# Performance work log

Measured on AMD Instinct MI355X. Metric: run time of the kernel, lower is better.

## Reference

```python
import jax, jax.numpy as jnp
import numpy as np
from jax import lax

NEG = -1e30  # safe -inf surrogate (avoids nan grads)
CTC_WEIGHT = 0.3


def _excl_cumsum(e):
    # exclusive cumsum along last axis: (..., U) -> (..., U+1)
    c = jnp.cumsum(e, axis=-1)
    return jnp.concatenate([jnp.zeros_like(c[..., :1]), c], axis=-1)


def _rnnt_loss(log_probs, targets, frame_len, tgt_len, blank):
    """RNNT forward DP. log_probs: (B,T,U+1,V) log-softmaxed. Returns per-seq NLL (B,)."""
    B, T, U1, V = log_probs.shape
    blank_lp = log_probs[..., blank]  # (B,T,U1)
    emit = jnp.take_along_axis(log_probs[:, :, :U1 - 1, :],
                               targets[:, None, :, None], axis=3)[..., 0]  # (B,T,U)
    # alpha[0,u] = sum_{j<u} emit[0,j]
    alpha0 = _excl_cumsum(emit[:, 0])  # (B,U1)

    def step(alpha_prev, inp):
        blank_prev, emit_t = inp  # (B,U1), (B,U)
        a = alpha_prev + blank_prev
        # alpha[t,u] = LSE(a_u, alpha[t,u-1] + emit[t,u-1]) solved in closed form:
        # alpha[t,u] = E[u] + cumLSE_{k<=u}(a_k - E[k]),  E = exclusive cumsum of emit
        E = _excl_cumsum(emit_t)
        alpha_t = E + lax.associative_scan(jnp.logaddexp, a - E, axis=-1)
        return alpha_t, alpha_t

    xs = (jnp.swapaxes(blank_lp[:, :-1], 0, 1), jnp.swapaxes(emit[:, 1:], 0, 1))
    _, alphas = lax.scan(step, alpha0, xs)
    alphas = jnp.concatenate([alpha0[None], alphas], axis=0)  # (T,B,U1)
    bi = jnp.arange(B)
    t_idx = frame_len - 1
    ll = alphas[t_idx, bi, tgt_len] + blank_lp[bi, t_idx, tgt_len]
    return -ll


def _ctc_loss(log_probs, targets, frame_len, tgt_len, blank):
    """CTC forward DP. log_probs: (B,T,V) log-softmaxed. Returns per-seq NLL (B,)."""
    B, T, V = log_probs.shape
    U = targets.shape[1]
    S = 2 * U + 1
    ext = jnp.full((B, S), blank, dtype=targets.dtype).at[:, 1::2].set(targets)  # (B,S)
    lp_ext = jnp.take_along_axis(log_probs, ext[:, None, :], axis=2)  # (B,T,S)
    ext_m2 = jnp.pad(ext[:, :-2], ((0, 0), (2, 0)), constant_values=blank)
    can_skip = (jnp.arange(S)[None, :] >= 2) & (ext != blank) & (ext != ext_m2)
    alpha0 = jnp.full((B, S), NEG).at[:, 0].set(lp_ext[:, 0, 0]).at[:, 1].set(lp_ext[:, 0, 1])

    def step(alpha, lp_t):
        p1 = jnp.pad(alpha[:, :-1], ((0, 0), (1, 0)), constant_values=NEG)
        p2 = jnp.where(can_skip,
                       jnp.pad(alpha[:, :-2], ((0, 0), (2, 0)), constant_values=NEG), NEG)
        m = jnp.maximum(jnp.maximum(alpha, p1), p2)
        new = lp_t + m + jnp.log(jnp.exp(alpha - m) + jnp.exp(p1 - m) + jnp.exp(p2 - m))
        return new, new

    _, alphas = lax.scan(step, alpha0, jnp.swapaxes(lp_ext, 0, 1)[1:])
    alphas = jnp.concatenate([alpha0[None], alphas], axis=0)  # (T,B,S)
    bi = jnp.arange(B)
    t_idx = frame_len - 1
    a_last = alphas[t_idx, bi, 2 * tgt_len]
    a_prev = alphas[t_idx, bi, 2 * tgt_len - 1]
    return -jnp.logaddexp(a_last, a_prev)


def setup_inputs() -> dict:
    key = jax.random.key(0)
    ks = jax.random.split(key, 9)
    B, T, U, V = 4, 200, 50, 1024
    D, H = 512, 640
    return {
        "x_enc": jax.random.normal(ks[0], (B, T, D), jnp.float32),
        "x_dec": jax.random.normal(ks[1], (B, U + 1, H), jnp.float32),
        "target": jax.random.randint(ks[2], (B, U), 0, V - 1),  # excludes blank = V-1
        "frame_length": jax.random.randint(ks[3], (B,), 150, T + 1).astype(jnp.int32),
        "target_length": jax.random.randint(ks[4], (B,), 30, U + 1).astype(jnp.int32),
        "W_ctc": jax.random.normal(ks[5], (D, V), jnp.float32) * 0.02,
        "b_ctc": jnp.zeros((V,), jnp.float32),
        "W_enc": jax.random.normal(ks[6], (D, H), jnp.float32) * 0.02,
        "W_pred": jax.random.normal(ks[7], (H, H), jnp.float32) * 0.02,
        "b_joint": jnp.zeros((H,), jnp.float32),
        "W_out": jax.random.normal(ks[8], (H, V), jnp.float32) * 0.02,
        "b_out": jnp.zeros((V,), jnp.float32),
    }


def reference(x_enc, x_dec, target, frame_length, target_length,
              W_ctc, b_ctc, W_enc, W_pred, b_joint, W_out, b_out):
    B = x_enc.shape[0]
    V = W_ctc.shape[1]
    blank = V - 1
    # CTC head: linear + log_softmax over vocab
    ctc_lp = jax.nn.log_softmax(x_enc @ W_ctc + b_ctc, axis=-1)  # (B,T,V)
    # Joiner: enc proj (B,T,1,J) + pred proj (B,1,U+1,J) -> tanh -> vocab
    joint = jnp.tanh(jnp.einsum('btd,dj->btj', x_enc, W_enc)[:, :, None, :]
                     + jnp.einsum('buh,hj->buj', x_dec, W_pred)[:, None, :, :]
                     + b_joint)  # (B,T,U+1,J)
    rnnt_lp = jax.nn.log_softmax(jnp.einsum('btuj,jv->btuv', joint, W_out) + b_out, axis=-1)
    rnnt = _rnnt_loss(rnnt_lp, target, frame_length, target_length, blank).mean()
    ctc = _ctc_loss(ctc_lp, target, frame_length, target_length, blank).sum() / B
    return rnnt + CTC_WEIGHT * ctc
```

## Files before the change

### kernel.cpp

```cpp
#include <hip/hip_runtime.h>
#include <hip/hip_bf16.h>

typedef __bf16 bf16_t;
typedef __attribute__((ext_vector_type(8))) __bf16 bf16x8;
typedef __attribute__((ext_vector_type(4))) float f32x4;
typedef __attribute__((ext_vector_type(8))) int i32x8;
typedef __attribute__((ext_vector_type(4))) int i32x4;

#define NEGV (-1e30f)

#define BB 4
#define TT 200
#define UU 50
#define U1 51
#define VV 1024
#define DD 512
#define HH 640
#define RTOT (BB*TT*U1)
#define RPAD 40832
#define NBLK 638
#define SS 101

__device__ __forceinline__ float lae(float a, float b) {
    float mx = fmaxf(a, b);
    return mx + __logf(__expf(a - mx) + __expf(b - mx));
}
__device__ __forceinline__ float lae3(float a, float b, float c) {
    float mx = fmaxf(fmaxf(a, b), c);
    return mx + __logf(__expf(a - mx) + __expf(b - mx) + __expf(c - mx));
}
__device__ __forceinline__ float tanh_fast(float x) {
    float ex = __expf(2.f * x);
    return 1.f - 2.f / (ex + 1.f);
}
__device__ __forceinline__ float tanh_rcp(float x) {
    x = fminf(fmaxf(x, -10.f), 10.f);
    float ex = __expf(2.f * x);
    float r = __builtin_amdgcn_rcpf(ex + 1.f);
    return (ex - 1.f) * r;
}

__device__ __forceinline__ void pack_seg(const float* __restrict__ W, bf16_t* __restrict__ Wf,
                                         int e, int K32, int N)
{
    int j  = e & 7;
    int l  = (e >> 3) & 63;
    int kk = (e >> 9) % K32;
    int nt = e / (K32 * 512);
    int v = nt * 16 + (l & 15);
    int k = kk * 32 + ((l >> 4) << 2) + (j & 3) + ((j >> 2) << 4);
    Wf[e] = (bf16_t)W[(size_t)k * N + v];
}

__device__ __forceinline__ void pack_out8_mx(const float* __restrict__ W, unsigned* __restrict__ Wf8,
                                             int e32)
{
    int w4   = e32 & 7;
    int l    = (e32 >> 3) & 63;
    int ksnt = e32 >> 9;
    int ks   = ksnt % 5;
    int nt   = ksnt / 5;
    int v = nt * 16 + (l & 15);
    int kb = ks * 128 + ((l >> 4) << 5) + w4 * 4;
    float f[4];
#pragma unroll
    for (int t = 0; t < 4; ++t) f[t] = W[(size_t)(kb + t) * VV + v] * 16.f;
    unsigned r = __builtin_amdgcn_cvt_pk_fp8_f32(f[0], f[1], 0, false);
    r = __builtin_amdgcn_cvt_pk_fp8_f32(f[2], f[3], r, true);
    Wf8[e32] = r;
}

__global__ void pack_all(const float* __restrict__ Wout, const float* __restrict__ Wenc,
                         const float* __restrict__ Wpred, const float* __restrict__ Wctc,
                         unsigned* __restrict__ FOut8, bf16_t* __restrict__ FEnc,
                         bf16_t* __restrict__ FPred, bf16_t* __restrict__ FCtc)
{
    int e = blockIdx.x * 256 + threadIdx.x;
    if (e < 163840) { pack_out8_mx(Wout, FOut8, e); return; }
    e -= 163840;
    if (e < 327680) { pack_seg(Wenc, FEnc, e, 16, 640); return; }
    e -= 327680;
    if (e < 409600) { pack_seg(Wpred, FPred, e, 20, 640); return; }
    e -= 409600;
    pack_seg(Wctc, FCtc, e, 16, 1024);
}

template<int K32, int L, bool LSE, int J>
__device__ void gemm_dev(const float* __restrict__ A, int M, int rowbase, int K,
                         const bf16_t* __restrict__ Wf, const float* __restrict__ bias,
                         float* __restrict__ C, float* __restrict__ lse_out, int N,
                         bf16_t* Atile, float (*ps)[8])
{
    const int tid = threadIdx.x;
#pragma unroll
    for (int it = 0; it < J * K32 / 8; ++it) {
        int fi = it * 512 + tid;
        int l = fi & 63, jk = fi >> 6;
        int j = jk / K32, kk = jk - j * K32;
        int row = rowbase + j * 16 + (l & 15);
        if (row > M - 1) row = M - 1;
        int c0 = kk * 32 + ((l >> 4) << 2);
        const float4 a0 = *(const float4*)&A[(size_t)row * K + c0];
        const float4 a1 = *(const float4*)&A[(size_t)row * K + c0 + 16];
        bf16x8 v;
        v[0] = (bf16_t)a0.x; v[1] = (bf16_t)a0.y; v[2] = (bf16_t)a0.z; v[3] = (bf16_t)a0.w;
        v[4] = (bf16_t)a1.x; v[5] = (bf16_t)a1.y; v[6] = (bf16_t)a1.z; v[7] = (bf16_t)a1.w;
        *(bf16x8*)&Atile[(size_t)fi * 8] = v;
    }
    __syncthreads();

    const int l = tid & 63, w = tid >> 6;
    const int lrow = l & 15, lhi = l >> 4;

    f32x4 acc[J][L];
#pragma unroll
    for (int j = 0; j < J; ++j)
#pragma unroll
        for (int li = 0; li < L; ++li) acc[j][li] = f32x4{0.f, 0.f, 0.f, 0.f};

    for (int kk = 0; kk < K32; ++kk) {
        bf16x8 a[J];
#pragma unroll
        for (int j = 0; j < J; ++j)
            a[j] = *(const bf16x8*)&Atile[(size_t)(((j * K32 + kk) * 64 + l) * 8)];
#pragma unroll
        for (int li = 0; li < L; ++li) {
            bf16x8 b = *(const bf16x8*)&Wf[(size_t)(((w * L + li) * K32 + kk) * 64 + l) * 8];
#pragma unroll
            for (int j = 0; j < J; ++j)
                acc[j][li] = __builtin_amdgcn_mfma_f32_16x16x32_bf16(a[j], b, acc[j][li], 0, 0, 0);
        }
    }

    float se[J][4];
    if (LSE) {
#pragma unroll
        for (int j = 0; j < J; ++j)
#pragma unroll
            for (int i = 0; i < 4; ++i) se[j][i] = 0.f;
    }
#pragma unroll
    for (int j = 0; j < J; ++j)
#pragma unroll
        for (int li = 0; li < L; ++li) {
            int col = (w * L + li) * 16 + lrow;
            float bv = bias ? bias[col] : 0.f;
#pragma unroll
            for (int i = 0; i < 4; ++i) {
                int grow = rowbase + 16 * j + lhi * 4 + i;
                float x = acc[j][li][i] + bv;
                if (grow < M) C[(size_t)grow * N + col] = x;
                if (LSE) se[j][i] += __expf(x);
            }
        }
    if (LSE) {
#pragma unroll
        for (int d = 1; d < 16; d <<= 1)
#pragma unroll
            for (int j = 0; j < J; ++j)
#pragma unroll
                for (int i = 0; i < 4; ++i) se[j][i] += __shfl_xor(se[j][i], d);
        if (lrow == 0) {
#pragma unroll
            for (int j = 0; j < J; ++j)
#pragma unroll
                for (int i = 0; i < 4; ++i) ps[16 * j + lhi * 4 + i][w] = se[j][i];
        }
        __syncthreads();
        if (tid < J * 16) {
            float s = 0.f;
#pragma unroll
            for (int w0 = 0; w0 < 8; ++w0) s += ps[tid][w0];
            int grow = rowbase + tid;
            if (grow < M) lse_out[grow] = __logf(s);
        }
    }
}

__global__ __launch_bounds__(512)
void mfma_gemm3(const float* __restrict__ x_enc, const float* __restrict__ x_dec,
                const bf16_t* __restrict__ FEnc, const bf16_t* __restrict__ FPred,
                const bf16_t* __restrict__ FCtc, const float* __restrict__ b_ctc,
                float* __restrict__ enc_proj, float* __restrict__ pred_proj,
                float* __restrict__ ctc_logits, float* __restrict__ ctc_lse)
{
    __shared__ bf16_t Atile[40960];
    __shared__ float ps[64][8];
    int blk = blockIdx.x;
    if (blk < 13)
        gemm_dev<16, 5, false, 4>(x_enc, 800, blk * 64, 512, FEnc, nullptr, enc_proj, nullptr, 640, Atile, ps);
    else if (blk < 17)
        gemm_dev<20, 5, false, 4>(x_dec, 204, (blk - 13) * 64, 640, FPred, nullptr, pred_proj, nullptr, 640, Atile, ps);
    else
        gemm_dev<16, 8, true, 4>(x_enc, 800, (blk - 17) * 64, 512, FCtc, b_ctc, ctc_logits, ctc_lse, 1024, Atile, ps);
}

__global__ __launch_bounds__(256)
void build_joint(const float* __restrict__ enc, const float* __restrict__ pred,
                 const float* __restrict__ bj, char* __restrict__ FA8)
{
    __shared__ __align__(16) char tile[64 * 656];
    __shared__ const float* ep[64];
    __shared__ const float* pp[64];
    const int blk = blockIdx.x;
    const int tid = threadIdx.x;

    if (tid < 64) {
        int r = blk * 64 + tid; if (r > RTOT - 1) r = RTOT - 1;
        int b = r / (TT * U1); int rem = r - b * (TT * U1);
        int t = rem / U1;      int u = rem - t * U1;
        ep[tid] = enc + (size_t)(b * TT + t) * HH;
        pp[tid] = pred + (size_t)(b * U1 + u) * HH;
    }
    __syncthreads();

#pragma unroll 4
    for (int it = 0; it < 40; ++it) {
        int i = it * 256 + tid;
        int row = i / 160;
        int c4 = i - row * 160;
        int c0 = c4 * 4;
        const float4 e4 = *(const float4*)&ep[row][c0];
        const float4 p4 = *(const float4*)&pp[row][c0];
        const float4 q4 = *(const float4*)&bj[c0];
        float f0 = tanh_rcp(e4.x + p4.x + q4.x);
        float f1 = tanh_rcp(e4.y + p4.y + q4.y);
        float f2 = tanh_rcp(e4.z + p4.z + q4.z);
        float f3 = tanh_rcp(e4.w + p4.w + q4.w);
        unsigned r0 = __builtin_amdgcn_cvt_pk_fp8_f32(f0, f1, 0, false);
        unsigned v = __builtin_amdgcn_cvt_pk_fp8_f32(f2, f3, r0, true);
        *(unsigned*)&tile[row * 656 + c0] = v;
    }
    __syncthreads();

#pragma unroll
    for (int it = 0; it < 10; ++it) {
        int c = it * 256 + tid;
        int lA = c & 63;
        int plane = c >> 6;
        int h = plane & 1;
        int jks = plane >> 1;
        int ks = jks % 5;
        int j = jks / 5;
        int row = j * 16 + (lA & 15);
        int kbase = ks * 128 + ((lA >> 4) << 5) + h * 16;
        uint4 v = *(const uint4*)&tile[row * 656 + kbase];
        *(uint4*)&FA8[(size_t)blk * 40960 + (size_t)c * 16] = v;
    }
}

__global__ __launch_bounds__(512)
void joint_gemm(const char* __restrict__ FA8,
                const unsigned* __restrict__ Wf8,
                const float* __restrict__ bo,
                const int* __restrict__ target,
                float* __restrict__ blank_buf, float* __restrict__ emit_buf)
{
    __shared__ __align__(16) char smbuf[40960];
    char* Afrag8 = smbuf;
    const int tid = threadIdx.x;
    const int blk = blockIdx.x;

    const int l = tid & 63, w = tid >> 6;
    const int lrow = l & 15, lhi = l >> 4;

    const uint4* src = (const uint4*)(FA8 + (size_t)blk * 40960);
#pragma unroll
    for (int it = 0; it < 5; ++it) {
        int c = it * 512 + tid;
        *(uint4*)&Afrag8[(size_t)c * 16] = src[c];
    }
    __syncthreads();

    f32x4 acc[4][8];
#pragma unroll
    for (int j = 0; j < 4; ++j)
#pragma unroll
        for (int li = 0; li < 8; ++li) acc[j][li] = f32x4{0.f, 0.f, 0.f, 0.f};

    const char* Bp8 = (const char*)Wf8 + (size_t)(w * 8) * 10240 + (size_t)l * 32;

    const int rot = blk % 5;
    auto kstep = [&](int ks) {
        i32x8 a[4];
#pragma unroll
        for (int j = 0; j < 4; ++j) {
            i32x4 lo = *(const i32x4*)(Afrag8 + (size_t)(((j * 5 + ks) * 2 + 0) * 1024 + l * 16));
            i32x4 hi = *(const i32x4*)(Afrag8 + (size_t)(((j * 5 + ks) * 2 + 1) * 1024 + l * 16));
            a[j][0] = lo[0]; a[j][1] = lo[1]; a[j][2] = lo[2]; a[j][3] = lo[3];
            a[j][4] = hi[0]; a[j][5] = hi[1]; a[j][6] = hi[2]; a[j][7] = hi[3];
        }
#pragma unroll
        for (int li = 0; li < 8; ++li) {
            i32x8 b = *(const i32x8*)(Bp8 + (size_t)li * 10240 + (size_t)ks * 2048);
#pragma unroll
            for (int j = 0; j < 4; ++j)
                acc[j][li] = __builtin_amdgcn_mfma_scale_f32_16x16x128_f8f6f4(
                    a[j], b, acc[j][li], 0, 0,
                    0, 0x7F7F7F7F, 0, 0x7F7F7F7F);
        }
    };
    for (int ks0 = rot; ks0 < 5; ++ks0) kstep(ks0);
    for (int ks0 = 0; ks0 < rot; ++ks0) kstep(ks0);

    int tg[4][4];
#pragma unroll
    for (int j = 0; j < 4; ++j)
#pragma unroll
        for (int i = 0; i < 4; ++i) {
            int r = blk * 64 + 16 * j + lhi * 4 + i; if (r > RTOT - 1) r = RTOT - 1;
            int b = r / (TT * U1); int rem = r - b * (TT * U1);
            int u = rem % U1;
            tg[j][i] = (u < UU) ? target[b * UU + u] : -1;
        }

    float se[4][4], ee[4][4], bbv[4][4];
#pragma unroll
    for (int j = 0; j < 4; ++j)
#pragma unroll
        for (int i = 0; i < 4; ++i) { se[j][i] = 0.f; ee[j][i] = NEGV; bbv[j][i] = NEGV; }

#pragma unroll
    for (int li = 0; li < 8; ++li) {
        int col = (w * 8 + li) * 16 + lrow;
        float bv = bo[col];
#pragma unroll
        for (int j = 0; j < 4; ++j)
#pragma unroll
            for (int i = 0; i < 4; ++i) {
                float x = acc[j][li][i] * 0.0625f + bv;
                se[j][i] += __expf(x);
                if (col == tg[j][i]) ee[j][i] = x;
            }
    }
    if (w == 7) {
        float bv = bo[1023];
#pragma unroll
        for (int j = 0; j < 4; ++j)
#pragma unroll
            for (int i = 0; i < 4; ++i) {
                float x = acc[j][7][i] * 0.0625f + bv;
                if (lrow == 15) bbv[j][i] = x;
            }
    }
#pragma unroll
    for (int d = 1; d < 16; d <<= 1)
#pragma unroll
        for (int j = 0; j < 4; ++j)
#pragma unroll
            for (int i = 0; i < 4; ++i) {
                se[j][i] += __shfl_xor(se[j][i], d);
                ee[j][i] = fmaxf(ee[j][i], __shfl_xor(ee[j][i], d));
                bbv[j][i] = fmaxf(bbv[j][i], __shfl_xor(bbv[j][i], d));
            }

    __syncthreads();
    float (*ps)[8] = (float (*)[8])(smbuf);
    float (*pe)[8] = (float (*)[8])(smbuf + 2048);
    float (*pb)[8] = (float (*)[8])(smbuf + 4096);
    if (lrow == 0) {
#pragma unroll
        for (int j = 0; j < 4; ++j)
#pragma unroll
            for (int i = 0; i < 4; ++i) {
                int r = 16 * j + lhi * 4 + i;
                ps[r][w] = se[j][i]; pe[r][w] = ee[j][i]; pb[r][w] = bbv[j][i];
            }
    }
    __syncthreads();
    if (tid < 64) {
        float s = 0.f, e = NEGV, bq = NEGV;
#pragma unroll
        for (int w0 = 0; w0 < 8; ++w0) {
            s += ps[tid][w0];
            e = fmaxf(e, pe[tid][w0]);
            bq = fmaxf(bq, pb[tid][w0]);
        }
        float lse = __logf(s);
        int gid = blk * 64 + tid;
        if (gid < RTOT) {
            blank_buf[gid] = bq - lse;
            emit_buf[gid]  = e - lse;
        }
    }
}

__global__ __launch_bounds__(256)
void dp_fused(const float* __restrict__ blank_buf, const float* __restrict__ emit_buf,
              const float* __restrict__ ctc_logits, const float* __restrict__ ctc_lse,
              const int* __restrict__ target, const int* __restrict__ frame_len,
              const int* __restrict__ tgt_len,
              float* __restrict__ out)
{
    __shared__ __align__(16) float sm[28416];
    const int bid = blockIdx.x;
    const int tid = threadIdx.x;

    if (bid < 4) {
        const int b = bid;
        float2* pk = (float2*)sm;
        for (int i = tid; i < TT * U1; i += 256) {
            int t = i / U1, uu = i - t * U1;
            float bl = blank_buf[(b * TT + t) * U1 + uu];
            float em = emit_buf[(b * TT + t) * U1 + uu];
            pk[uu * 217 + t + 8] = make_float2(bl, em);
        }
        __syncthreads();
        if (tid >= 64) return;
        const int u = tid;
        const int fl = frame_len[b], tl = tgt_len[b];
        const int dh = fl - 1 + tl;
        const bool isTL = (u == tl);
        const bool act = (u < U1);
        float A = (u == 0) ? 0.f : NEGV;
        float Asave = (dh == 0 && isTL) ? A : NEGV;
        const float2* prow = pk + u * 217;

        for (int d0 = 1; d0 <= 249; d0 += 8) {
            int tb = d0 - 1 - u;
            int tc = tb; if (tc < -8) tc = -8; if (tc > 200) tc = 200;
            float2 buf[8];
#pragma unroll
            for (int s = 0; s < 8; ++s) buf[s] = prow[tc + 8 + s];
#pragma unroll
            for (int s = 0; s < 8; ++s) {
                int d = d0 + s;
                int t_new = d - u;
                float2 be = buf[s];
                float vshare = A + be.y;
                float left = __shfl_up(vshare, 1);
                if (u == 0) left = NEGV;
                float up = (t_new >= 1) ? (A + be.x) : NEGV;
                float Anew = lae(up, left);
                bool valid = act && (t_new >= 0) && (t_new < TT);
                A = valid ? Anew : A;
                Asave = (isTL && d == dh) ? A : Asave;
            }
        }
        if (isTL && act) {
            float bl = prow[(fl - 1) + 8].x;
            atomicAdd(out, -0.25f * (Asave + bl));
        }
    } else {
        const int b = bid - 4;
        float* lpE = sm;
        float* lpO = sm + 208;
        for (int i = tid; i < TT; i += 256) {
            int bt = b * TT + i;
            lpE[i] = ctc_logits[(size_t)bt * VV + (VV - 1)] - ctc_lse[bt];
        }
        for (int i = tid; i < TT * UU; i += 256) {
            int t = i / UU, uu = i - t * UU;
            int bt = b * TT + t;
            lpO[uu * 209 + t] = ctc_logits[(size_t)bt * VV + target[b * UU + uu]] - ctc_lse[bt];
        }
        __syncthreads();
        if (tid >= 64) return;
        const int u = tid;
        const int fl = frame_len[b], tl = tgt_len[b];
        const bool acte = (u <= 50);
        const bool acto = (u < 50);
        bool skip = (u >= 1 && u < UU) ? (target[b * UU + u] != target[b * UU + u - 1]) : false;
        const float* orow = lpO + u * 209;
        float old_e = (u == 0) ? lpE[0] : NEGV;
        float old_o = (u == 0) ? orow[0] : NEGV;
        float Esave = (fl == 1) ? old_e : NEGV;
        float Osave = (fl == 1) ? old_o : NEGV;

        for (int t0 = 1; t0 <= 193; t0 += 8) {
            float bo8[8], be8[8];
#pragma unroll
            for (int s = 0; s < 8; ++s) { bo8[s] = orow[t0 + s]; be8[s] = lpE[t0 + s]; }
#pragma unroll
            for (int s = 0; s < 8; ++s) {
                int t = t0 + s;
                float prev_o = __shfl_up(old_o, 1);
                if (u == 0) prev_o = NEGV;
                float ne = be8[s] + lae(old_e, prev_o);
                float no = bo8[s] + lae3(old_o, old_e, skip ? prev_o : NEGV);
                old_e = acte ? ne : NEGV;
                old_o = acto ? no : NEGV;
                bool hv = (t == fl - 1) && (t < TT);
                Esave = hv ? old_e : Esave;
                Osave = hv ? old_o : Osave;
            }
        }
        float a_last = __shfl(Esave, tl);
        float a_prev = __shfl(Osave, tl - 1);
        if (u == 0) atomicAdd(out, -0.075f * lae(a_last, a_prev));
    }
}

extern "C" void kernel_launch(void* const* d_in, const int* in_sizes, int n_in,
                              void* d_out, int out_size, void* d_ws, size_t ws_size,
                              hipStream_t stream)
{
    const float* x_enc   = (const float*)d_in[0];
    const float* x_dec   = (const float*)d_in[1];
    const int*   target  = (const int*)d_in[2];
    const int*   frame_l = (const int*)d_in[3];
    const int*   tgt_l   = (const int*)d_in[4];
    const float* W_ctc   = (const float*)d_in[5];
    const float* b_ctc   = (const float*)d_in[6];
    const float* W_enc   = (const float*)d_in[7];
    const float* W_pred  = (const float*)d_in[8];
    const float* b_joint = (const float*)d_in[9];
    const float* W_out   = (const float*)d_in[10];
    const float* b_out   = (const float*)d_in[11];
    float* out = (float*)d_out;

    float* wsf        = (float*)d_ws;
    float* enc_proj   = wsf;
    float* pred_proj  = wsf + 512000;
    float* ctc_logits = wsf + 642560;
    float* ctc_lse    = wsf + 1461760;
    float* blank_buf  = wsf + 1462592;
    float* emit_buf   = wsf + 1503424;
    unsigned* FOut8 = (unsigned*)(wsf + 1544272);
    bf16_t* FEnc  = (bf16_t*)(wsf + 1708112);
    bf16_t* FPred = (bf16_t*)(wsf + 1871952);
    bf16_t* FCtc  = (bf16_t*)(wsf + 2076752);
    char*   FA8   = (char*)(wsf + 2338896);

    hipMemsetAsync(out, 0, sizeof(float), stream);
    pack_all<<<5568, 256, 0, stream>>>(W_out, W_enc, W_pred, W_ctc, FOut8, FEnc, FPred, FCtc);
    mfma_gemm3<<<30, 512, 0, stream>>>(x_enc, x_dec, FEnc, FPred, FCtc, b_ctc,
                                       enc_proj, pred_proj, ctc_logits, ctc_lse);
    build_joint<<<NBLK, 256, 0, stream>>>(enc_proj, pred_proj, b_joint, FA8);
    joint_gemm<<<NBLK, 512, 0, stream>>>(FA8, FOut8, b_out, target, blank_buf, emit_buf);
    dp_fused<<<8, 256, 0, stream>>>(blank_buf, emit_buf, ctc_logits, ctc_lse,
                                    target, frame_l, tgt_l, out);
}
```

Measured before the change: 164.5 us.

## Split small GEMMs into more blocks and overlap fp8 W_out packing with them

```diff
diff --git a/kernel.cpp b/kernel.cpp
--- a/kernel.cpp
+++ b/kernel.cpp
@@ -17,7 +17,6 @@
 #define DD 512
 #define HH 640
 #define RTOT (BB*TT*U1)
-#define RPAD 40832
 #define NBLK 638
 #define SS 101
 
@@ -28,10 +27,6 @@
 __device__ __forceinline__ float lae3(float a, float b, float c) {
     float mx = fmaxf(fmaxf(a, b), c);
     return mx + __logf(__expf(a - mx) + __expf(b - mx) + __expf(c - mx));
-}
-__device__ __forceinline__ float tanh_fast(float x) {
-    float ex = __expf(2.f * x);
-    return 1.f - 2.f / (ex + 1.f);
 }
 __device__ __forceinline__ float tanh_rcp(float x) {
     x = fminf(fmaxf(x, -10.f), 10.f);
@@ -70,14 +65,13 @@
     Wf8[e32] = r;
 }
 
-__global__ void pack_all(const float* __restrict__ Wout, const float* __restrict__ Wenc,
-                         const float* __restrict__ Wpred, const float* __restrict__ Wctc,
-                         unsigned* __restrict__ FOut8, bf16_t* __restrict__ FEnc,
-                         bf16_t* __restrict__ FPred, bf16_t* __restrict__ FCtc)
-{
+__global__ void pack_bf16(const float* __restrict__ Wenc, const float* __restrict__ Wpred,
+                          const float* __restrict__ Wctc,
+                          bf16_t* __restrict__ FEnc, bf16_t* __restrict__ FPred,
+                          bf16_t* __restrict__ FCtc, float* __restrict__ out)
+{
+    if (blockIdx.x == 0 && threadIdx.x == 0) out[0] = 0.f;
     int e = blockIdx.x * 256 + threadIdx.x;
-    if (e < 163840) { pack_out8_mx(Wout, FOut8, e); return; }
-    e -= 163840;
     if (e < 327680) { pack_seg(Wenc, FEnc, e, 16, 640); return; }
     e -= 327680;
     if (e < 409600) { pack_seg(Wpred, FPred, e, 20, 640); return; }
@@ -182,20 +176,26 @@
                 const bf16_t* __restrict__ FEnc, const bf16_t* __restrict__ FPred,
                 const bf16_t* __restrict__ FCtc, const float* __restrict__ b_ctc,
                 float* __restrict__ enc_proj, float* __restrict__ pred_proj,
-                float* __restrict__ ctc_logits, float* __restrict__ ctc_lse)
-{
-    __shared__ bf16_t Atile[40960];
+                float* __restrict__ ctc_logits, float* __restrict__ ctc_lse,
+                const float* __restrict__ Wout, unsigned* __restrict__ FOut8)
+{
+    __shared__ bf16_t Atile[2560 * 8];
     __shared__ float ps[64][8];
     int blk = blockIdx.x;
-    if (blk < 13)
-        gemm_dev<16, 5, false, 4>(x_enc, 800, blk * 64, 512, FEnc, nullptr, enc_proj, nullptr, 640, Atile, ps);
-    else if (blk < 17)
-        gemm_dev<20, 5, false, 4>(x_dec, 204, (blk - 13) * 64, 640, FPred, nullptr, pred_proj, nullptr, 640, Atile, ps);
+    if (blk >= 107) {
+        int e = (blk - 107) * 512 + threadIdx.x;
+        pack_out8_mx(Wout, FOut8, e);
+        return;
+    }
+    if (blk < 50)
+        gemm_dev<16, 5, false, 1>(x_enc, 800, blk * 16, 512, FEnc, nullptr, enc_proj, nullptr, 640, Atile, ps);
+    else if (blk < 57)
+        gemm_dev<20, 5, false, 2>(x_dec, 204, (blk - 50) * 32, 640, FPred, nullptr, pred_proj, nullptr, 640, Atile, ps);
     else
-        gemm_dev<16, 8, true, 4>(x_enc, 800, (blk - 17) * 64, 512, FCtc, b_ctc, ctc_logits, ctc_lse, 1024, Atile, ps);
-}
-
-__global__ __launch_bounds__(256)
+        gemm_dev<16, 8, true, 1>(x_enc, 800, (blk - 57) * 16, 512, FCtc, b_ctc, ctc_logits, ctc_lse, 1024, Atile, ps);
+}
+
+__global__ __launch_bounds__(512)
 void build_joint(const float* __restrict__ enc, const float* __restrict__ pred,
                  const float* __restrict__ bj, char* __restrict__ FA8)
 {
@@ -215,8 +215,8 @@
     __syncthreads();
 
 #pragma unroll 4
-    for (int it = 0; it < 40; ++it) {
-        int i = it * 256 + tid;
+    for (int it = 0; it < 20; ++it) {
+        int i = it * 512 + tid;
         int row = i / 160;
         int c4 = i - row * 160;
         int c0 = c4 * 4;
@@ -234,8 +234,8 @@
     __syncthreads();
 
 #pragma unroll
-    for (int it = 0; it < 10; ++it) {
-        int c = it * 256 + tid;
+    for (int it = 0; it < 5; ++it) {
+        int c = it * 512 + tid;
         int lA = c & 63;
         int plane = c >> 6;
         int h = plane & 1;
@@ -522,11 +522,11 @@
     bf16_t* FCtc  = (bf16_t*)(wsf + 2076752);
     char*   FA8   = (char*)(wsf + 2338896);
 
-    hipMemsetAsync(out, 0, sizeof(float), stream);
-    pack_all<<<5568, 256, 0, stream>>>(W_out, W_enc, W_pred, W_ctc, FOut8, FEnc, FPred, FCtc);
-    mfma_gemm3<<<30, 512, 0, stream>>>(x_enc, x_dec, FEnc, FPred, FCtc, b_ctc,
-                                       enc_proj, pred_proj, ctc_logits, ctc_lse);
-    build_joint<<<NBLK, 256, 0, stream>>>(enc_proj, pred_proj, b_joint, FA8);
+    pack_bf16<<<4928, 256, 0, stream>>>(W_enc, W_pred, W_ctc, FEnc, FPred, FCtc, out);
+    mfma_gemm3<<<427, 512, 0, stream>>>(x_enc, x_dec, FEnc, FPred, FCtc, b_ctc,
+                                        enc_proj, pred_proj, ctc_logits, ctc_lse,
+                                        W_out, FOut8);
+    build_joint<<<NBLK, 512, 0, stream>>>(enc_proj, pred_proj, b_joint, FA8);
     joint_gemm<<<NBLK, 512, 0, stream>>>(FA8, FOut8, b_out, target, blank_buf, emit_buf);
     dp_fused<<<8, 256, 0, stream>>>(blank_buf, emit_buf, ctc_logits, ctc_lse,
                                     target, frame_l, tgt_l, out);
```

Result: faster. 152.4 us (-7.4%).
